# Performance work log

Measured on AMD Instinct MI355X. Metric: run time of the kernel, lower is better.

Reference implementation:

```python
import jax, jax.numpy as jnp
import numpy as np

NEG_INF = -1e30  # log-semiring zero
B, T, D, V, L = 16, 800, 512, 5000, 100


def setup_inputs() -> dict:
    key = jax.random.key(0)
    k1, k2, k3, k4, k5, k6 = jax.random.split(key, 6)
    hs_pad = jax.random.normal(k1, (B, T, D), dtype=jnp.float32)
    W = jax.random.normal(k2, (D, V), dtype=jnp.float32) / np.sqrt(D)
    b = jnp.zeros((V,), dtype=jnp.float32)
    hlens = jax.random.randint(k3, (B,), T // 2, T + 1, dtype=jnp.int32)
    labels = jax.random.randint(k4, (B, L), 1, V, dtype=jnp.int32)  # blank=0 excluded
    label_lens = jax.random.randint(k5, (B,), L // 2, L + 1, dtype=jnp.int32)
    return {"hs_pad": hs_pad, "W": W, "b": b, "hlens": hlens,
            "labels": labels, "label_lens": label_lens}


def _ctc_tot_scores(log_probs, hlens, labels, label_lens):
    # Standard CTC log-semiring forward DP (equivalent to k2 CTC-topology
    # intersect_dense + get_tot_scores). log_probs: [B,T,V], blank id = 0.
    Bb, Tt, Vv = log_probs.shape
    Ll = labels.shape[1]
    S = 2 * Ll + 1  # extended sequence: blank, l1, blank, l2, ..., blank
    ext = jnp.zeros((Bb, S), dtype=labels.dtype).at[:, 1::2].set(labels)
    # skip transition (s-2 -> s) allowed iff ext[s] != blank and ext[s] != ext[s-2]
    skip = jnp.concatenate(
        [jnp.zeros((Bb, 2), dtype=bool),
         (ext[:, 2:] != ext[:, :-2]) & (ext[:, 2:] != 0)], axis=1)
    # emissions along extended labels: lp_ext[b,t,s] = log_probs[b,t,ext[b,s]]
    lp_ext = jax.vmap(lambda lp, e: lp[:, e])(log_probs, ext)  # [B,T,S]
    alpha = jnp.full((Bb, S), NEG_INF, dtype=log_probs.dtype)
    alpha = alpha.at[:, 0].set(lp_ext[:, 0, 0])
    alpha = alpha.at[:, 1].set(lp_ext[:, 0, 1])

    def step(alpha, inp):
        t, lp_t = inp  # lp_t: [B,S]
        prev1 = jnp.pad(alpha[:, :-1], ((0, 0), (1, 0)), constant_values=NEG_INF)
        prev2 = jnp.pad(alpha[:, :-2], ((0, 0), (2, 0)), constant_values=NEG_INF)
        prev2 = jnp.where(skip, prev2, NEG_INF)
        a = jnp.logaddexp(jnp.logaddexp(alpha, prev1), prev2) + lp_t
        # freeze rows whose sequence has ended (t >= hlen)
        return jnp.where((t < hlens)[:, None], a, alpha), None

    ts = jnp.arange(1, Tt)
    alpha, _ = jax.lax.scan(step, alpha, (ts, jnp.swapaxes(lp_ext, 0, 1)[1:]))
    last = 2 * label_lens  # index of final blank per utterance
    a_last = jnp.take_along_axis(alpha, last[:, None], axis=1)[:, 0]
    a_prev = jnp.take_along_axis(alpha, (last - 1)[:, None], axis=1)[:, 0]
    return jnp.logaddexp(a_last, a_prev)  # [B] total log-likelihoods


def reference(hs_pad, W, b, hlens, labels, label_lens):
    # ctc_lo Linear (dropout_rate=0 -> identity) + log_softmax
    logits = jnp.einsum('btd,dv->btv', hs_pad, W) + b
    log_probs = jax.nn.log_softmax(logits, axis=-1)
    tot = _ctc_tot_scores(log_probs, hlens, labels, label_lens)
    # forward_scores = -tot_scores, reduce=True -> mean
    return jnp.mean(-tot)
```

## Files before the change

### kernel.cpp

```cpp
#include <hip/hip_runtime.h>

#define NEG_INF -1e30f

typedef __attribute__((ext_vector_type(8))) __bf16 bf16x8;
typedef __attribute__((ext_vector_type(4))) float f32x4;

constexpr int Bb = 16, T = 800, D = 512, V = 5000, L = 100;
constexpr int ROWS = Bb * T;
constexpr int S = 2 * L + 1;
constexpr int SP = 208;
constexpr int VP = 5120;
constexpr int NCB = VP / 128;
constexpr int NRB = ROWS / 128;
constexpr int NGB = Bb * 50;
constexpr int CONVB = ROWS * D / 1024;
constexpr int RSTRIDE = SP * 4;
constexpr int CH = 8;
constexpr int CHB = 7168;

static __device__ __forceinline__ unsigned short f2bf(float x) {
  union { float f; unsigned u; } v; v.f = x;
  unsigned r = (v.u + 0x7FFFu + ((v.u >> 16) & 1u)) >> 16;
  return (unsigned short)r;
}

static __device__ __forceinline__ double dpp_shr1_zero_d(double x) {
  long long b = __double_as_longlong(x);
  int lo = (int)(b & 0xFFFFFFFFLL);
  int hi = (int)(b >> 32);
  int nlo = __builtin_amdgcn_update_dpp(0, lo, 0x138, 0xF, 0xF, false);
  int nhi = __builtin_amdgcn_update_dpp(0, hi, 0x138, 0xF, 0xF, false);
  return __longlong_as_double(((long long)(unsigned)nlo) | ((long long)nhi << 32));
}
static __device__ __forceinline__ double dpp_shl1_zero_d(double x) {
  long long b = __double_as_longlong(x);
  int lo = (int)(b & 0xFFFFFFFFLL);
  int hi = (int)(b >> 32);
  int nlo = __builtin_amdgcn_update_dpp(0, lo, 0x130, 0xF, 0xF, false);
  int nhi = __builtin_amdgcn_update_dpp(0, hi, 0x130, 0xF, 0xF, false);
  return __longlong_as_double(((long long)(unsigned)nlo) | ((long long)nhi << 32));
}

static __device__ __forceinline__ float ex2(float x) { return __builtin_amdgcn_exp2f(x); }
static __device__ __forceinline__ float lg2(float x) { return __builtin_amdgcn_logf(x); }

static __device__ __forceinline__ float lg2d(double z) {
  long long b = __double_as_longlong(z);
  int e = (int)((b >> 52) & 0x7FF);
  if (e == 0) return -1.0e30f;
  unsigned mant = (unsigned)((b >> 29) & 0x7FFFFFu);
  float mf = __int_as_float(0x3F800000u | mant);
  return (float)(e - 1023) + lg2(mf);
}

__global__ __launch_bounds__(256) void k_prep(const float* __restrict__ hs,
                                              const float* __restrict__ W,
                                              unsigned short* __restrict__ A,
                                              unsigned short* __restrict__ Wt) {
  __shared__ float tile[64][65];
  int blk = blockIdx.x;
  if (blk < CONVB) {
    int i = blk * 256 + threadIdx.x;
    float4 f = ((const float4*)hs)[i];
    ushort4 o;
    o.x = f2bf(f.x); o.y = f2bf(f.y); o.z = f2bf(f.z); o.w = f2bf(f.w);
    ((ushort4*)A)[i] = o;
    return;
  }
  int g = blk - CONVB;
  int v0 = (g % (VP / 64)) * 64, k0 = (g / (VP / 64)) * 64;
  int tl = threadIdx.x & 63, th = threadIdx.x >> 6;
#pragma unroll
  for (int i = 0; i < 16; i++) {
    int k = k0 + th + i * 4;
    int v = v0 + tl;
    tile[th + i * 4][tl] = (v < V) ? W[(size_t)k * V + v] : 0.f;
  }
  __syncthreads();
#pragma unroll
  for (int i = 0; i < 16; i++) {
    int v = v0 + th + i * 4;
    int k = k0 + tl;
    Wt[(size_t)v * D + k] = f2bf(tile[tl][th + i * 4]);
  }
}

__global__ __launch_bounds__(256) void k_gather(const unsigned short* __restrict__ A,
                                                const unsigned short* __restrict__ Wt,
                                                const float* __restrict__ bias,
                                                const int* __restrict__ labels,
                                                float* __restrict__ glog) {
  int tid = threadIdx.x;
  int lane = tid & 63, w = tid >> 6;
  int q = lane >> 4, c = lane & 15;
  int b = blockIdx.x & 15, chk = blockIdx.x >> 4;
  int t0 = chk * 16;
  int bT = b * T, bL = b * L;
  int st0 = (w == 0) ? 0 : 4 + (w - 1) * 3;
  int nst = (w == 0) ? 4 : 3;

  int evs[4]; float bvs[4];
#pragma unroll
  for (int j = 0; j < 4; j++) {
    int st = st0 + (j < nst ? j : nst - 1);
    int s = st * 16 + c;
    evs[j] = (s < S && (s & 1)) ? labels[bL + (s >> 1)] : 0;
    bvs[j] = bias[evs[j]];
  }
  const unsigned short* Arow = A + (size_t)(bT + t0 + c) * D;
  f32x4 acc[4];
#pragma unroll
  for (int j = 0; j < 4; j++) acc[j] = (f32x4){0.f, 0.f, 0.f, 0.f};
  for (int kk = 0; kk < D; kk += 32) {
    bf16x8 aa = *(const bf16x8*)(Arow + kk + q * 8);
#pragma unroll
    for (int j = 0; j < 4; j++) {
      bf16x8 bb = *(const bf16x8*)(Wt + (size_t)evs[j] * D + kk + q * 8);
      acc[j] = __builtin_amdgcn_mfma_f32_16x16x32_bf16(aa, bb, acc[j], 0, 0, 0);
    }
  }
#pragma unroll
  for (int j = 0; j < 4; j++) {
    if (j >= nst) break;
    int st = st0 + j;
#pragma unroll
    for (int r = 0; r < 4; r++)
      glog[(size_t)(bT + t0 + q * 4 + r) * SP + st * 16 + c] = acc[j][r] + bvs[j];
  }
}

#define RENORM4(A0, A1, A2, A3, KC) {                                           \
    long long ba0 = __double_as_longlong(A0), ba1 = __double_as_longlong(A1);   \
    long long ba2 = __double_as_longlong(A2), ba3 = __double_as_longlong(A3);   \
    int ee0 = (int)((ba0 >> 52) & 0x7FF), ee1 = (int)((ba1 >> 52) & 0x7FF);     \
    int ee2 = (int)((ba2 >> 52) & 0x7FF), ee3 = (int)((ba3 >> 52) & 0x7FF);     \
    int em = ee0 > ee1 ? ee0 : ee1;                                             \
    em = em > ee2 ? em : ee2;                                                   \
    em = em > ee3 ? em : ee3;                                                   \
    _Pragma("unroll")                                                           \
    for (int o = 1; o < 64; o <<= 1) { int q2 = __shfl_xor(em, o); em = em > q2 ? em : q2; } \
    if (em > 0 && em < 2046) {                                                  \
      double sc = __longlong_as_double((long long)(2046 - em) << 52);           \
      A0 *= sc; A1 *= sc; A2 *= sc; A3 *= sc;                                   \
      KC += em - 1023;                                                          \
    } }

__global__ __launch_bounds__(256) void k_fused(const unsigned short* __restrict__ A,
                                               const unsigned short* __restrict__ Wt,
                                               const float* __restrict__ bias,
                                               const float* __restrict__ glog,
                                               const int* __restrict__ labels,
                                               const int* __restrict__ hlens,
                                               const int* __restrict__ llens,
                                               float* __restrict__ partM,
                                               float* __restrict__ partS,
                                               float* __restrict__ rawtot) {
  __shared__ __attribute__((aligned(16))) char smem[34816];

  int blk = blockIdx.x;
  if (blk < Bb) {
    int tid = threadIdx.x;
    int w = tid >> 6, l = tid & 63;
    if (w >= 2) { __syncthreads(); return; }

    int b = blk;
    int col4 = ((4 * l < SP) ? 4 * l : SP - 4) * 4;
    const char* gvb = (const char*)glog + (size_t)b * T * RSTRIDE;
    int hl = hlens[b];
    int mfw = (hl - 1) >> 1;
    const size_t gmax = (size_t)T * RSTRIDE - 16;

    int i0 = (2 * l < L) ? 2 * l : L - 1;
    int i1 = (2 * l + 1 < L) ? 2 * l + 1 : L - 1;
    int im = (l >= 1) ? 2 * l - 1 : 0; im = im < L ? im : L - 1;
    int lab0 = labels[b * L + i0];
    int lab1 = labels[b * L + i1];
    int labm = labels[b * L + im];
    bool sk1 = (l >= 1) && (lab0 != 0) && (lab0 != labm);
    bool sk3 = (lab1 != 0) && (lab1 != lab0);

    constexpr float LOG2E = 1.44269504f;
    float* laf = (float*)(smem + 28672);
    float* lbf = (float*)(smem + 29504);

    if (w == 0) {
      f32x4 g0 = *(const f32x4*)(gvb + col4);
      double z0 = (l == 0) ? 1.0 : 0.0;
      double z1 = (l == 0) ? (double)ex2((g0.y - g0.x) * LOG2E) : 0.0;
      double z2 = 0.0, z3 = 0.0;
      double Csum = (double)g0.x;
      int Kc = 0;

      auto stageF = [&](int cc, int dst) {
        size_t sb = (size_t)(1 + cc * CH) * RSTRIDE;
#pragma unroll
        for (int pg = 0; pg < 7; pg++) {
          size_t ob = sb + (size_t)pg * 1024 + (size_t)l * 16;
          if (ob > gmax) ob = gmax;
          __builtin_amdgcn_global_load_lds(
              (const __attribute__((address_space(1))) void*)(gvb + ob),
              (__attribute__((address_space(3))) void*)(smem + dst * CHB + pg * 1024),
              16, 0, 0);
        }
      };

#define FW_STEPZ(G) {                                                  \
    float e1f = ex2(((G).y - (G).x) * LOG2E);                          \
    float e3f = ex2(((G).w - (G).x) * LOG2E);                          \
    Csum += (double)(G).x;                                             \
    double p3 = dpp_shr1_zero_d(z3);                                   \
    double nz0 = z0 + p3;                                              \
    double nz1 = (z1 + z0 + (sk1 ? p3 : 0.0)) * (double)e1f;           \
    double nz2 = z2 + z1;                                              \
    double nz3 = (z3 + z2 + (sk3 ? z1 : 0.0)) * (double)e3f;           \
    z0 = nz0; z1 = nz1; z2 = nz2; z3 = nz3; }

      int nchF = (mfw + CH - 1) / CH;
      stageF(0, 0);
      stageF(1, 1);
      for (int c = 0; c < nchF; ++c) {
        int cur = c & 1;
        if (c + 2 < nchF) { asm volatile("s_waitcnt vmcnt(7)" ::: "memory"); }
        else             { asm volatile("s_waitcnt vmcnt(0)" ::: "memory"); }
        __builtin_amdgcn_sched_barrier(0);
        const char* bufc = smem + cur * CHB + col4;
        int steps = mfw - c * CH; if (steps > CH) steps = CH;
        if (steps == CH) {
          f32x4 G[8];
#pragma unroll
          for (int j = 0; j < 8; j++) G[j] = *(const f32x4*)(bufc + j * RSTRIDE);
#pragma unroll
          for (int j = 0; j < 8; j++) FW_STEPZ(G[j])
          RENORM4(z0, z1, z2, z3, Kc)
        } else {
          for (int j = 0; j < steps; j++) {
            f32x4 G = *(const f32x4*)(bufc + j * RSTRIDE);
            FW_STEPZ(G)
          }
        }
        if (c + 2 < nchF) {
          asm volatile("s_waitcnt lgkmcnt(0)" ::: "memory");
          stageF(c + 2, cur);
        }
      }
#undef FW_STEPZ
      if (l < 52) {
        float base = (float)(Csum * 1.4426950408889634 + (double)Kc);
        laf[4 * l + 0] = base + lg2d(z0);
        laf[4 * l + 1] = base + lg2d(z1);
        laf[4 * l + 2] = base + lg2d(z2);
        laf[4 * l + 3] = base + lg2d(z3);
      }
    } else {
      int ll = llens[b];
      int sA = 2 * ll, sB = sA - 1;
      int s0i = 4 * l;
      double b0 = (s0i == sA || s0i == sB) ? 1.0 : 0.0;
      double b1 = (s0i + 1 == sA || s0i + 1 == sB) ? 1.0 : 0.0;
      double b2 = (s0i + 2 == sA || s0i + 2 == sB) ? 1.0 : 0.0;
      double b3 = (s0i + 3 == sA || s0i + 3 == sB) ? 1.0 : 0.0;
      double Csum = 0.0;
      int Kc = 0;
      int sk1i = sk1 ? 1 : 0;
      bool sk1n = __shfl_down(sk1i, 1) != 0;

      auto stageB = [&](int cc, int dst) {
        int rlo = hl - 1 - cc * CH - 7;
        size_t sb = (size_t)rlo * RSTRIDE;
#pragma unroll
        for (int pg = 0; pg < 7; pg++) {
          size_t ob = sb + (size_t)pg * 1024 + (size_t)l * 16;
          if (ob > gmax) ob = gmax;
          __builtin_amdgcn_global_load_lds(
              (const __attribute__((address_space(1))) void*)(gvb + ob),
              (__attribute__((address_space(3))) void*)(smem + dst * CHB + pg * 1024),
              16, 0, 0);
        }
      };

#define BW_STEPZ(G) {                                                  \
    float e1f = ex2(((G).y - (G).x) * LOG2E);                          \
    float e3f = ex2(((G).w - (G).x) * LOG2E);                          \
    Csum += (double)(G).x;                                             \
    double f1 = b1 * (double)e1f;                                      \
    double f3 = b3 * (double)e3f;                                      \
    double q4 = dpp_shl1_zero_d(b0);                                   \
    double q5 = dpp_shl1_zero_d(f1);                                   \
    double nb0 = b0 + f1;                                              \
    double nb1 = f1 + b2 + (sk3 ? f3 : 0.0);                           \
    double nb2 = b2 + f3;                                              \
    double nb3 = f3 + q4 + (sk1n ? q5 : 0.0);                          \
    b0 = nb0; b1 = nb1; b2 = nb2; b3 = nb3; }

      int bsteps = (hl - 1) - mfw;
      int nchB = (bsteps + CH - 1) / CH;
      stageB(0, 2);
      stageB(1, 3);
      for (int c = 0; c < nchB; ++c) {
        int cur = c & 1;
        if (c + 2 < nchB) { asm volatile("s_waitcnt vmcnt(7)" ::: "memory"); }
        else             { asm volatile("s_waitcnt vmcnt(0)" ::: "memory"); }
        __builtin_amdgcn_sched_barrier(0);
        const char* bufc = smem + (2 + cur) * CHB + col4;
        int hi = hl - 1 - c * CH;
        int steps = hi - mfw; if (steps > CH) steps = CH;
        if (steps == CH) {
          f32x4 G[8];
#pragma unroll
          for (int j = 0; j < 8; j++) G[j] = *(const f32x4*)(bufc + (7 - j) * RSTRIDE);
#pragma unroll
          for (int j = 0; j < 8; j++) BW_STEPZ(G[j])
          RENORM4(b0, b1, b2, b3, Kc)
        } else {
          for (int j = 0; j < steps; j++) {
            f32x4 G = *(const f32x4*)(bufc + (7 - j) * RSTRIDE);
            BW_STEPZ(G)
          }
        }
        if (c + 2 < nchB) {
          asm volatile("s_waitcnt lgkmcnt(0)" ::: "memory");
          stageB(c + 2, 2 + cur);
        }
      }
#undef BW_STEPZ
      if (l < 52) {
        float base = (float)(Csum * 1.4426950408889634 + (double)Kc);
        lbf[4 * l + 0] = base + lg2d(b0);
        lbf[4 * l + 1] = base + lg2d(b1);
        lbf[4 * l + 2] = base + lg2d(b2);
        lbf[4 * l + 3] = base + lg2d(b3);
      }
    }

    __syncthreads();
    if (w == 0) {
      float v[4];
#pragma unroll
      for (int r = 0; r < 4; r++) {
        int s = 4 * l + r;
        v[r] = (l < 52 && s < S) ? (laf[s] + lbf[s]) : -1.0e30f;
      }
      float mx = fmaxf(fmaxf(v[0], v[1]), fmaxf(v[2], v[3]));
#pragma unroll
      for (int o = 1; o < 64; o <<= 1) mx = fmaxf(mx, __shfl_xor(mx, o));
      float ssum = ex2(v[0] - mx) + ex2(v[1] - mx) + ex2(v[2] - mx) + ex2(v[3] - mx);
#pragma unroll
      for (int o = 1; o < 64; o <<= 1) ssum += __shfl_xor(ssum, o);
      if (l == 0)
        rawtot[b] = 0.6931471805599453f * (mx + lg2(ssum));
    }
    return;
  }

  unsigned short* As = (unsigned short*)smem;
  unsigned short* Bs = (unsigned short*)(smem + 16384);
  float (*redM)[128] = (float (*)[128])(smem + 32768);
  float (*redS)[128] = (float (*)[128])(smem + 33792);

  int gblk = blk - Bb;
  int cb = gblk % NCB, rb = gblk / NCB;
  int tid = threadIdx.x;
  int lane = tid & 63, w = tid >> 6;
  int q = lane >> 4, c = lane & 15;
  int mh = w & 1, nh = w >> 1;
  int row0 = rb * 128, n0 = cb * 128;
  int lr = lane >> 3, lc = lane & 7;
  int oc = (lc ^ lr) * 8;

  f32x4 acc[4][4];
#pragma unroll
  for (int mt = 0; mt < 4; mt++)
#pragma unroll
    for (int nt = 0; nt < 4; nt++) acc[mt][nt] = (f32x4){0.f, 0.f, 0.f, 0.f};

  for (int kk = 0; kk < D; kk += 64) {
#pragma unroll
    for (int j = 0; j < 4; j++) {
      int i = w * 4 + j;
      const unsigned short* ga = A + (size_t)(row0 + i * 8 + lr) * D + kk + oc;
      __builtin_amdgcn_global_load_lds(
          (const __attribute__((address_space(1))) void*)ga,
          (__attribute__((address_space(3))) void*)(As + i * 512), 16, 0, 0);
      const unsigned short* gb = Wt + (size_t)(n0 + i * 8 + lr) * D + kk + oc;
      __builtin_amdgcn_global_load_lds(
          (const __attribute__((address_space(1))) void*)gb,
          (__attribute__((address_space(3))) void*)(Bs + i * 512), 16, 0, 0);
    }
    __syncthreads();
#pragma unroll
    for (int kq = 0; kq < 2; kq++) {
      int o = ((kq * 4 + q) ^ (c & 7)) * 8;
      bf16x8 af[4], bfr[4];
#pragma unroll
      for (int mt = 0; mt < 4; mt++)
        af[mt] = *(const bf16x8*)(As + (mh * 64 + mt * 16 + c) * 64 + o);
#pragma unroll
      for (int nt = 0; nt < 4; nt++)
        bfr[nt] = *(const bf16x8*)(Bs + (nh * 64 + nt * 16 + c) * 64 + o);
#pragma unroll
      for (int mt = 0; mt < 4; mt++)
#pragma unroll
        for (int nt = 0; nt < 4; nt++)
          acc[mt][nt] = __builtin_amdgcn_mfma_f32_16x16x32_bf16(af[mt], bfr[nt], acc[mt][nt], 0, 0, 0);
    }
    __syncthreads();
  }

  int vcb[4]; float bv[4];
#pragma unroll
  for (int nt = 0; nt < 4; nt++) {
    vcb[nt] = n0 + nh * 64 + nt * 16 + c;
    bv[nt] = (vcb[nt] < V) ? bias[vcb[nt]] : 0.f;
  }
#pragma unroll
  for (int mt = 0; mt < 4; mt++) {
#pragma unroll
    for (int r = 0; r < 4; r++) {
      float x[4]; float m = NEG_INF;
#pragma unroll
      for (int nt = 0; nt < 4; nt++) {
        x[nt] = (vcb[nt] < V) ? (acc[mt][nt][r] + bv[nt]) : NEG_INF;
        m = fmaxf(m, x[nt]);
      }
#pragma unroll
      for (int o = 1; o < 16; o <<= 1) m = fmaxf(m, __shfl_xor(m, o));
      float s = 0.f;
#pragma unroll
      for (int nt = 0; nt < 4; nt++) s += __expf(x[nt] - m);
#pragma unroll
      for (int o = 1; o < 16; o <<= 1) s += __shfl_xor(s, o);
      if (c == 0) {
        int rloc = mh * 64 + mt * 16 + q * 4 + r;
        redM[nh][rloc] = m;
        redS[nh][rloc] = s;
      }
    }
  }
  __syncthreads();
  if (tid < 128) {
    float m0 = redM[0][tid], m1 = redM[1][tid];
    float mm = fmaxf(m0, m1);
    float ss = redS[0][tid] * __expf(m0 - mm) + redS[1][tid] * __expf(m1 - mm);
    partM[(size_t)cb * ROWS + row0 + tid] = mm;
    partS[(size_t)cb * ROWS + row0 + tid] = ss;
  }
}

__global__ __launch_bounds__(256) void k_lse(const float* __restrict__ pM,
                                             const float* __restrict__ pS,
                                             float* __restrict__ lse) {
  int row = blockIdx.x * 256 + threadIdx.x;
  float m = pM[row], s = pS[row];
  for (int cb = 1; cb < NCB; cb++) {
    float M2 = pM[(size_t)cb * ROWS + row], S2 = pS[(size_t)cb * ROWS + row];
    float mn = fmaxf(m, M2);
    s = s * __expf(m - mn) + S2 * __expf(M2 - mn);
    m = mn;
  }
  lse[row] = m + __logf(s);
}

__global__ __launch_bounds__(1024) void k_final(const float* __restrict__ lse,
                                                const float* __restrict__ rawtot,
                                                const int* __restrict__ hlens,
                                                float* __restrict__ out) {
  __shared__ float acc[Bb];
  int w = threadIdx.x >> 6, l = threadIdx.x & 63;
  int hl = hlens[w];
  float s = 0.f;
  for (int t = l; t < hl; t += 64) s += lse[w * T + t];
#pragma unroll
  for (int o = 1; o < 64; o <<= 1) s += __shfl_xor(s, o);
  if (l == 0) acc[w] = rawtot[w] - s;
  __syncthreads();
  if (threadIdx.x == 0) {
    float m = 0.f;
    for (int i = 0; i < Bb; i++) m += acc[i];
    out[0] = -m / (float)Bb;
  }
}

extern "C" void kernel_launch(void* const* d_in, const int* in_sizes, int n_in,
                              void* d_out, int out_size, void* d_ws, size_t ws_size,
                              hipStream_t stream) {
  const float* hs    = (const float*)d_in[0];
  const float* W     = (const float*)d_in[1];
  const float* bias  = (const float*)d_in[2];
  const int* hlens   = (const int*)d_in[3];
  const int* labels  = (const int*)d_in[4];
  const int* llens   = (const int*)d_in[5];
  float* out = (float*)d_out;

  char* ws = (char*)d_ws;
  unsigned short* A    = (unsigned short*)(ws);
  unsigned short* Wt   = (unsigned short*)(ws + 13107200);
  float*          partM= (float*)(ws + 18350080);
  float*          partS= (float*)(ws + 20398080);
  float*          lse  = (float*)(ws + 22446080);
  float*          glog = (float*)(ws + 22497280);
  float*          rawtot=(float*)(ws + 33146880);

  k_prep<<<CONVB + (VP / 64) * (D / 64), 256, 0, stream>>>(hs, W, A, Wt);
  k_gather<<<NGB, 256, 0, stream>>>(A, Wt, bias, labels, glog);
  k_fused<<<Bb + NCB * NRB, 256, 0, stream>>>(A, Wt, bias, glog, labels, hlens, llens,
                                              partM, partS, rawtot);
  k_lse<<<ROWS / 256, 256, 0, stream>>>(partM, partS, lse);
  k_final<<<1, 1024, 0, stream>>>(lse, rawtot, hlens, out);

  (void)in_sizes; (void)n_in; (void)out_size; (void)ws_size;
}
```

Baseline: 262.6 us.

## Split CTC DP into its own kernel, double chunk size, shorten backward dependency chain

Moves the per-utterance forward/backward CTC recursion out of the fused GEMM/log-softmax kernel into a separate 128-thread k_dp kernel launched on the same stream before k_fused. The DP chunk staged into LDS grows from 8 to 16 frames, with matching waitcnt and staging counts. In the backward step, the lane shift is now applied to b1 and e1f separately, so the shift no longer waits on the product f1. The split frees the GEMM kernel from the DP's shared-memory footprint and branch. It gives up the concurrency the DP blocks previously had with the GEMM blocks, so the serial DP latency may now add directly to total time.

```diff
diff --git a/kernel.cpp b/kernel.cpp
--- a/kernel.cpp
+++ b/kernel.cpp
@@ -15,8 +15,8 @@
 constexpr int NGB = Bb * 50;
 constexpr int CONVB = ROWS * D / 1024;
 constexpr int RSTRIDE = SP * 4;
-constexpr int CH = 8;
-constexpr int CHB = 7168;
+constexpr int CH = 16;
+constexpr int CHB = CH * RSTRIDE;
 
 static __device__ __forceinline__ unsigned short f2bf(float x) {
   union { float f; unsigned u; } v; v.f = x;
@@ -39,6 +39,10 @@
   int nlo = __builtin_amdgcn_update_dpp(0, lo, 0x130, 0xF, 0xF, false);
   int nhi = __builtin_amdgcn_update_dpp(0, hi, 0x130, 0xF, 0xF, false);
   return __longlong_as_double(((long long)(unsigned)nlo) | ((long long)nhi << 32));
+}
+static __device__ __forceinline__ float dpp_shl1_zero_f(float x) {
+  return __int_as_float(__builtin_amdgcn_update_dpp(
+      0, __float_as_int(x), 0x130, 0xF, 0xF, false));
 }
 
 static __device__ __forceinline__ float ex2(float x) { return __builtin_amdgcn_exp2f(x); }
@@ -145,64 +149,55 @@
       KC += em - 1023;                                                          \
     } }
 
-__global__ __launch_bounds__(256) void k_fused(const unsigned short* __restrict__ A,
-                                               const unsigned short* __restrict__ Wt,
-                                               const float* __restrict__ bias,
-                                               const float* __restrict__ glog,
-                                               const int* __restrict__ labels,
-                                               const int* __restrict__ hlens,
-                                               const int* __restrict__ llens,
-                                               float* __restrict__ partM,
-                                               float* __restrict__ partS,
-                                               float* __restrict__ rawtot) {
-  __shared__ __attribute__((aligned(16))) char smem[34816];
-
-  int blk = blockIdx.x;
-  if (blk < Bb) {
-    int tid = threadIdx.x;
-    int w = tid >> 6, l = tid & 63;
-    if (w >= 2) { __syncthreads(); return; }
-
-    int b = blk;
-    int col4 = ((4 * l < SP) ? 4 * l : SP - 4) * 4;
-    const char* gvb = (const char*)glog + (size_t)b * T * RSTRIDE;
-    int hl = hlens[b];
-    int mfw = (hl - 1) >> 1;
-    const size_t gmax = (size_t)T * RSTRIDE - 16;
-
-    int i0 = (2 * l < L) ? 2 * l : L - 1;
-    int i1 = (2 * l + 1 < L) ? 2 * l + 1 : L - 1;
-    int im = (l >= 1) ? 2 * l - 1 : 0; im = im < L ? im : L - 1;
-    int lab0 = labels[b * L + i0];
-    int lab1 = labels[b * L + i1];
-    int labm = labels[b * L + im];
-    bool sk1 = (l >= 1) && (lab0 != 0) && (lab0 != labm);
-    bool sk3 = (lab1 != 0) && (lab1 != lab0);
-
-    constexpr float LOG2E = 1.44269504f;
-    float* laf = (float*)(smem + 28672);
-    float* lbf = (float*)(smem + 29504);
-
-    if (w == 0) {
-      f32x4 g0 = *(const f32x4*)(gvb + col4);
-      double z0 = (l == 0) ? 1.0 : 0.0;
-      double z1 = (l == 0) ? (double)ex2((g0.y - g0.x) * LOG2E) : 0.0;
-      double z2 = 0.0, z3 = 0.0;
-      double Csum = (double)g0.x;
-      int Kc = 0;
-
-      auto stageF = [&](int cc, int dst) {
-        size_t sb = (size_t)(1 + cc * CH) * RSTRIDE;
-#pragma unroll
-        for (int pg = 0; pg < 7; pg++) {
-          size_t ob = sb + (size_t)pg * 1024 + (size_t)l * 16;
-          if (ob > gmax) ob = gmax;
-          __builtin_amdgcn_global_load_lds(
-              (const __attribute__((address_space(1))) void*)(gvb + ob),
-              (__attribute__((address_space(3))) void*)(smem + dst * CHB + pg * 1024),
-              16, 0, 0);
-        }
-      };
+__global__ __launch_bounds__(128) void k_dp(const float* __restrict__ glog,
+                                            const int* __restrict__ labels,
+                                            const int* __restrict__ hlens,
+                                            const int* __restrict__ llens,
+                                            float* __restrict__ rawtot) {
+  __shared__ __attribute__((aligned(16))) char smem[54912];
+  int tid = threadIdx.x;
+  int w = tid >> 6, l = tid & 63;
+  int b = blockIdx.x;
+
+  int col4 = ((4 * l < SP) ? 4 * l : SP - 4) * 4;
+  const char* gvb = (const char*)glog + (size_t)b * T * RSTRIDE;
+  int hl = hlens[b];
+  int mfw = (hl - 1) >> 1;
+  const size_t gmax = (size_t)T * RSTRIDE - 16;
+
+  int i0 = (2 * l < L) ? 2 * l : L - 1;
+  int i1 = (2 * l + 1 < L) ? 2 * l + 1 : L - 1;
+  int im = (l >= 1) ? 2 * l - 1 : 0; im = im < L ? im : L - 1;
+  int lab0 = labels[b * L + i0];
+  int lab1 = labels[b * L + i1];
+  int labm = labels[b * L + im];
+  bool sk1 = (l >= 1) && (lab0 != 0) && (lab0 != labm);
+  bool sk3 = (lab1 != 0) && (lab1 != lab0);
+
+  constexpr float LOG2E = 1.44269504f;
+  float* laf = (float*)(smem + 53248);
+  float* lbf = (float*)(smem + 54080);
+
+  if (w == 0) {
+    f32x4 g0 = *(const f32x4*)(gvb + col4);
+    double z0 = (l == 0) ? 1.0 : 0.0;
+    double z1 = (l == 0) ? (double)ex2((g0.y - g0.x) * LOG2E) : 0.0;
+    double z2 = 0.0, z3 = 0.0;
+    double Csum = (double)g0.x;
+    int Kc = 0;
+
+    auto stageF = [&](int cc, int dst) {
+      size_t sb = (size_t)(1 + cc * CH) * RSTRIDE;
+#pragma unroll
+      for (int pg = 0; pg < 13; pg++) {
+        size_t ob = sb + (size_t)pg * 1024 + (size_t)l * 16;
+        if (ob > gmax) ob = gmax;
+        __builtin_amdgcn_global_load_lds(
+            (const __attribute__((address_space(1))) void*)(gvb + ob),
+            (__attribute__((address_space(3))) void*)(smem + dst * CHB + pg * 1024),
+            16, 0, 0);
+      }
+    };
 
 #define FW_STEPZ(G) {                                                  \
     float e1f = ex2(((G).y - (G).x) * LOG2E);                          \
@@ -215,149 +210,163 @@
     double nz3 = (z3 + z2 + (sk3 ? z1 : 0.0)) * (double)e3f;           \
     z0 = nz0; z1 = nz1; z2 = nz2; z3 = nz3; }
 
-      int nchF = (mfw + CH - 1) / CH;
-      stageF(0, 0);
-      stageF(1, 1);
-      for (int c = 0; c < nchF; ++c) {
-        int cur = c & 1;
-        if (c + 2 < nchF) { asm volatile("s_waitcnt vmcnt(7)" ::: "memory"); }
-        else             { asm volatile("s_waitcnt vmcnt(0)" ::: "memory"); }
-        __builtin_amdgcn_sched_barrier(0);
-        const char* bufc = smem + cur * CHB + col4;
-        int steps = mfw - c * CH; if (steps > CH) steps = CH;
-        if (steps == CH) {
-          f32x4 G[8];
-#pragma unroll
-          for (int j = 0; j < 8; j++) G[j] = *(const f32x4*)(bufc + j * RSTRIDE);
-#pragma unroll
-          for (int j = 0; j < 8; j++) FW_STEPZ(G[j])
-          RENORM4(z0, z1, z2, z3, Kc)
-        } else {
-          for (int j = 0; j < steps; j++) {
-            f32x4 G = *(const f32x4*)(bufc + j * RSTRIDE);
-            FW_STEPZ(G)
-          }
+    int nchF = (mfw + CH - 1) / CH;
+    stageF(0, 0);
+    stageF(1, 1);
+    for (int c = 0; c < nchF; ++c) {
+      int cur = c & 1;
+      if (c + 2 < nchF) { asm volatile("s_waitcnt vmcnt(13)" ::: "memory"); }
+      else             { asm volatile("s_waitcnt vmcnt(0)" ::: "memory"); }
+      __builtin_amdgcn_sched_barrier(0);
+      const char* bufc = smem + cur * CHB + col4;
+      int steps = mfw - c * CH; if (steps > CH) steps = CH;
+      if (steps == CH) {
+        f32x4 G[8];
+#pragma unroll
+        for (int j = 0; j < 8; j++) G[j] = *(const f32x4*)(bufc + j * RSTRIDE);
+#pragma unroll
+        for (int j = 0; j < 8; j++) FW_STEPZ(G[j])
+#pragma unroll
+        for (int j = 0; j < 8; j++) G[j] = *(const f32x4*)(bufc + (8 + j) * RSTRIDE);
+#pragma unroll
+        for (int j = 0; j < 8; j++) FW_STEPZ(G[j])
+        RENORM4(z0, z1, z2, z3, Kc)
+      } else {
+        for (int j = 0; j < steps; j++) {
+          f32x4 G = *(const f32x4*)(bufc + j * RSTRIDE);
+          FW_STEPZ(G)
         }
-        if (c + 2 < nchF) {
-          asm volatile("s_waitcnt lgkmcnt(0)" ::: "memory");
-          stageF(c + 2, cur);
-        }
-      }
+      }
+      if (c + 2 < nchF) {
+        asm volatile("s_waitcnt lgkmcnt(0)" ::: "memory");
+        stageF(c + 2, cur);
+      }
+    }
 #undef FW_STEPZ
-      if (l < 52) {
-        float base = (float)(Csum * 1.4426950408889634 + (double)Kc);
-        laf[4 * l + 0] = base + lg2d(z0);
-        laf[4 * l + 1] = base + lg2d(z1);
-        laf[4 * l + 2] = base + lg2d(z2);
-        laf[4 * l + 3] = base + lg2d(z3);
-      }
-    } else {
-      int ll = llens[b];
-      int sA = 2 * ll, sB = sA - 1;
-      int s0i = 4 * l;
-      double b0 = (s0i == sA || s0i == sB) ? 1.0 : 0.0;
-      double b1 = (s0i + 1 == sA || s0i + 1 == sB) ? 1.0 : 0.0;
-      double b2 = (s0i + 2 == sA || s0i + 2 == sB) ? 1.0 : 0.0;
-      double b3 = (s0i + 3 == sA || s0i + 3 == sB) ? 1.0 : 0.0;
-      double Csum = 0.0;
-      int Kc = 0;
-      int sk1i = sk1 ? 1 : 0;
-      bool sk1n = __shfl_down(sk1i, 1) != 0;
-
-      auto stageB = [&](int cc, int dst) {
-        int rlo = hl - 1 - cc * CH - 7;
-        size_t sb = (size_t)rlo * RSTRIDE;
-#pragma unroll
-        for (int pg = 0; pg < 7; pg++) {
-          size_t ob = sb + (size_t)pg * 1024 + (size_t)l * 16;
-          if (ob > gmax) ob = gmax;
-          __builtin_amdgcn_global_load_lds(
-              (const __attribute__((address_space(1))) void*)(gvb + ob),
-              (__attribute__((address_space(3))) void*)(smem + dst * CHB + pg * 1024),
-              16, 0, 0);
-        }
-      };
+    if (l < 52) {
+      float base = (float)(Csum * 1.4426950408889634 + (double)Kc);
+      laf[4 * l + 0] = base + lg2d(z0);
+      laf[4 * l + 1] = base + lg2d(z1);
+      laf[4 * l + 2] = base + lg2d(z2);
+      laf[4 * l + 3] = base + lg2d(z3);
+    }
+  } else {
+    int ll = llens[b];
+    int sA = 2 * ll, sB = sA - 1;
+    int s0i = 4 * l;
+    double b0 = (s0i == sA || s0i == sB) ? 1.0 : 0.0;
+    double b1 = (s0i + 1 == sA || s0i + 1 == sB) ? 1.0 : 0.0;
+    double b2 = (s0i + 2 == sA || s0i + 2 == sB) ? 1.0 : 0.0;
+    double b3 = (s0i + 3 == sA || s0i + 3 == sB) ? 1.0 : 0.0;
+    double Csum = 0.0;
+    int Kc = 0;
+    int sk1i = sk1 ? 1 : 0;
+    bool sk1n = __shfl_down(sk1i, 1) != 0;
+
+    auto stageB = [&](int cc, int dst) {
+      int rlo = hl - 1 - cc * CH - 15;
+      size_t sb = (size_t)rlo * RSTRIDE;
+#pragma unroll
+      for (int pg = 0; pg < 13; pg++) {
+        size_t ob = sb + (size_t)pg * 1024 + (size_t)l * 16;
+        if (ob > gmax) ob = gmax;
+        __builtin_amdgcn_global_load_lds(
+            (const __attribute__((address_space(1))) void*)(gvb + ob),
+            (__attribute__((address_space(3))) void*)(smem + dst * CHB + pg * 1024),
+            16, 0, 0);
+      }
+    };
 
 #define BW_STEPZ(G) {                                                  \
     float e1f = ex2(((G).y - (G).x) * LOG2E);                          \
     float e3f = ex2(((G).w - (G).x) * LOG2E);                          \
+    float e1s = dpp_shl1_zero_f(e1f);                                  \
     Csum += (double)(G).x;                                             \
+    double b1s = dpp_shl1_zero_d(b1);                                  \
+    double q4  = dpp_shl1_zero_d(b0);                                  \
     double f1 = b1 * (double)e1f;                                      \
     double f3 = b3 * (double)e3f;                                      \
-    double q4 = dpp_shl1_zero_d(b0);                                   \
-    double q5 = dpp_shl1_zero_d(f1);                                   \
+    double q5 = b1s * (double)e1s;                                     \
     double nb0 = b0 + f1;                                              \
     double nb1 = f1 + b2 + (sk3 ? f3 : 0.0);                           \
     double nb2 = b2 + f3;                                              \
     double nb3 = f3 + q4 + (sk1n ? q5 : 0.0);                          \
     b0 = nb0; b1 = nb1; b2 = nb2; b3 = nb3; }
 
-      int bsteps = (hl - 1) - mfw;
-      int nchB = (bsteps + CH - 1) / CH;
-      stageB(0, 2);
-      stageB(1, 3);
-      for (int c = 0; c < nchB; ++c) {
-        int cur = c & 1;
-        if (c + 2 < nchB) { asm volatile("s_waitcnt vmcnt(7)" ::: "memory"); }
-        else             { asm volatile("s_waitcnt vmcnt(0)" ::: "memory"); }
-        __builtin_amdgcn_sched_barrier(0);
-        const char* bufc = smem + (2 + cur) * CHB + col4;
-        int hi = hl - 1 - c * CH;
-        int steps = hi - mfw; if (steps > CH) steps = CH;
-        if (steps == CH) {
-          f32x4 G[8];
-#pragma unroll
-          for (int j = 0; j < 8; j++) G[j] = *(const f32x4*)(bufc + (7 - j) * RSTRIDE);
-#pragma unroll
-          for (int j = 0; j < 8; j++) BW_STEPZ(G[j])
-          RENORM4(b0, b1, b2, b3, Kc)
-        } else {
-          for (int j = 0; j < steps; j++) {
-            f32x4 G = *(const f32x4*)(bufc + (7 - j) * RSTRIDE);
-            BW_STEPZ(G)
-          }
+    int bsteps = (hl - 1) - mfw;
+    int nchB = (bsteps + CH - 1) / CH;
+    stageB(0, 2);
+    stageB(1, 3);
+    for (int c = 0; c < nchB; ++c) {
+      int cur = c & 1;
+      if (c + 2 < nchB) { asm volatile("s_waitcnt vmcnt(13)" ::: "memory"); }
+      else             { asm volatile("s_waitcnt vmcnt(0)" ::: "memory"); }
+      __builtin_amdgcn_sched_barrier(0);
+      const char* bufc = smem + (2 + cur) * CHB + col4;
+      int hi = hl - 1 - c * CH;
+      int steps = hi - mfw; if (steps > CH) steps = CH;
+      if (steps == CH) {
+        f32x4 G[8];
+#pragma unroll
+        for (int j = 0; j < 8; j++) G[j] = *(const f32x4*)(bufc + (15 - j) * RSTRIDE);
+#pragma unroll
+        for (int j = 0; j < 8; j++) BW_STEPZ(G[j])
+#pragma unroll
+        for (int j = 0; j < 8; j++) G[j] = *(const f32x4*)(bufc + (7 - j) * RSTRIDE);
+#pragma unroll
+        for (int j = 0; j < 8; j++) BW_STEPZ(G[j])
+        RENORM4(b0, b1, b2, b3, Kc)
+      } else {
+        for (int j = 0; j < steps; j++) {
+          f32x4 G = *(const f32x4*)(bufc + (15 - j) * RSTRIDE);
+          BW_STEPZ(G)
         }
-        if (c + 2 < nchB) {
-          asm volatile("s_waitcnt lgkmcnt(0)" ::: "memory");
-          stageB(c + 2, 2 + cur);
-        }
-      }
+      }
+      if (c + 2 < nchB) {
+        asm volatile("s_waitcnt lgkmcnt(0)" ::: "memory");
+        stageB(c + 2, 2 + cur);
+      }
+    }
 #undef BW_STEPZ
-      if (l < 52) {
-        float base = (float)(Csum * 1.4426950408889634 + (double)Kc);
-        lbf[4 * l + 0] = base + lg2d(b0);
-        lbf[4 * l + 1] = base + lg2d(b1);
-        lbf[4 * l + 2] = base + lg2d(b2);
-        lbf[4 * l + 3] = base + lg2d(b3);
-      }
-    }
-
-    __syncthreads();
-    if (w == 0) {
-      float v[4];
-#pragma unroll
-      for (int r = 0; r < 4; r++) {
-        int s = 4 * l + r;
-        v[r] = (l < 52 && s < S) ? (laf[s] + lbf[s]) : -1.0e30f;
-      }
-      float mx = fmaxf(fmaxf(v[0], v[1]), fmaxf(v[2], v[3]));
-#pragma unroll
-      for (int o = 1; o < 64; o <<= 1) mx = fmaxf(mx, __shfl_xor(mx, o));
-      float ssum = ex2(v[0] - mx) + ex2(v[1] - mx) + ex2(v[2] - mx) + ex2(v[3] - mx);
-#pragma unroll
-      for (int o = 1; o < 64; o <<= 1) ssum += __shfl_xor(ssum, o);
-      if (l == 0)
-        rawtot[b] = 0.6931471805599453f * (mx + lg2(ssum));
-    }
-    return;
-  }
-
-  unsigned short* As = (unsigned short*)smem;
-  unsigned short* Bs = (unsigned short*)(smem + 16384);
-  float (*redM)[128] = (float (*)[128])(smem + 32768);
-  float (*redS)[128] = (float (*)[128])(smem + 33792);
-
-  int gblk = blk - Bb;
+    if (l < 52) {
+      float base = (float)(Csum * 1.4426950408889634 + (double)Kc);
+      lbf[4 * l + 0] = base + lg2d(b0);
+      lbf[4 * l + 1] = base + lg2d(b1);
+      lbf[4 * l + 2] = base + lg2d(b2);
+      lbf[4 * l + 3] = base + lg2d(b3);
+    }
+  }
+
+  __syncthreads();
+  if (w == 0) {
+    float v[4];
+#pragma unroll
+    for (int r = 0; r < 4; r++) {
+      int s = 4 * l + r;
+      v[r] = (l < 52 && s < S) ? (laf[s] + lbf[s]) : -1.0e30f;
+    }
+    float mx = fmaxf(fmaxf(v[0], v[1]), fmaxf(v[2], v[3]));
+#pragma unroll
+    for (int o = 1; o < 64; o <<= 1) mx = fmaxf(mx, __shfl_xor(mx, o));
+    float ssum = ex2(v[0] - mx) + ex2(v[1] - mx) + ex2(v[2] - mx) + ex2(v[3] - mx);
+#pragma unroll
+    for (int o = 1; o < 64; o <<= 1) ssum += __shfl_xor(ssum, o);
+    if (l == 0)
+      rawtot[b] = 0.6931471805599453f * (mx + lg2(ssum));
+  }
+}
+
+__global__ __launch_bounds__(256) void k_fused(const unsigned short* __restrict__ A,
+                                               const unsigned short* __restrict__ Wt,
+                                               const float* __restrict__ bias,
+                                               float* __restrict__ partM,
+                                               float* __restrict__ partS) {
+  __shared__ unsigned short As[128 * 64];
+  __shared__ unsigned short Bs[128 * 64];
+  __shared__ float redM[2][128];
+  __shared__ float redS[2][128];
+
+  int gblk = blockIdx.x;
   int cb = gblk % NCB, rb = gblk / NCB;
   int tid = threadIdx.x;
   int lane = tid & 63, w = tid >> 6;
@@ -502,8 +511,8 @@
 
   k_prep<<<CONVB + (VP / 64) * (D / 64), 256, 0, stream>>>(hs, W, A, Wt);
   k_gather<<<NGB, 256, 0, stream>>>(A, Wt, bias, labels, glog);
-  k_fused<<<Bb + NCB * NRB, 256, 0, stream>>>(A, Wt, bias, glog, labels, hlens, llens,
-                                              partM, partS, rawtot);
+  k_dp<<<Bb, 128, 0, stream>>>(glog, labels, hlens, llens, rawtot);
+  k_fused<<<NCB * NRB, 256, 0, stream>>>(A, Wt, bias, partM, partS);
   k_lse<<<ROWS / 256, 256, 0, stream>>>(partM, partS, lse);
   k_final<<<1, 1024, 0, stream>>>(lse, rawtot, hlens, out);
 
```

After: 303.3 us. 15.5% more time.
